# Kernel tuning notes

Measured on AMD Instinct MI355X. Metric: run time of the kernel, lower is better.

The kernel has to match this reference:

```python
import jax, jax.numpy as jnp
import numpy as np

D_MODEL = 512
H = 8
DEPTH = D_MODEL // H
TOPK = 16
TAU_HID = max(4, D_MODEL // 2)  # 256
TAU_EPS = 1e-6
DT = 1.0
T_SCALAR = 1.0  # default t in call()


def setup_inputs() -> dict:
    key = jax.random.key(0)
    ks = jax.random.split(key, 24)
    B, T = 2, 1024
    D2 = 2 * DEPTH

    def w(k, shape, fan_in):
        return jax.random.normal(k, shape, dtype=jnp.float32) / np.sqrt(fan_in)

    inp = {
        "x": jax.random.normal(ks[0], (B, T, D_MODEL), dtype=jnp.float32),
        "Wq": w(ks[1], (D_MODEL, D_MODEL), D_MODEL), "bq": jnp.zeros((D_MODEL,), jnp.float32),
        "Wk": w(ks[2], (D_MODEL, D_MODEL), D_MODEL), "bk": jnp.zeros((D_MODEL,), jnp.float32),
        "Wv": w(ks[3], (D_MODEL, D_MODEL), D_MODEL), "bv": jnp.zeros((D_MODEL,), jnp.float32),
        "Wo": w(ks[4], (D_MODEL, D_MODEL), D_MODEL), "bo": jnp.zeros((D_MODEL,), jnp.float32),
        "Wpi": w(ks[5], (D2, D_MODEL), D2), "bpi": jnp.zeros((D_MODEL,), jnp.float32),
        "Wpo": w(ks[6], (D_MODEL, 1), D_MODEL), "bpo": jnp.zeros((1,), jnp.float32),
        "Wta": w(ks[7], (D2, 1), D2), "bta": jnp.zeros((1,), jnp.float32),
        "Wtb": w(ks[8], (D2, 1), D2), "btb": jnp.zeros((1,), jnp.float32),
        "Wti": w(ks[9], (D2, TAU_HID), D2), "bti": jnp.zeros((TAU_HID,), jnp.float32),
        "Wto": w(ks[10], (TAU_HID, 1), TAU_HID), "bto": jnp.zeros((1,), jnp.float32),
    }
    return inp


def reference(x, Wq, bq, Wk, bk, Wv, bv, Wo, bo,
              Wpi, bpi, Wpo, bpo, Wta, bta, Wtb, btb, Wti, bti, Wto, bto):
    B, T, _ = x.shape

    def split_heads(z):
        return z.reshape(B, T, H, DEPTH).transpose(0, 2, 1, 3)  # [B,H,T,D]

    qh = split_heads(x @ Wq + bq)
    kh = split_heads(x @ Wk + bk)
    vh = split_heads(x @ Wv + bv)

    # top-k pairwise scores (q @ k^T), select K keys per query
    scores = jnp.einsum('bhqd,bhkd->bhqk', qh, kh)  # [B,H,T,T]
    _, idx = jax.lax.top_k(scores, TOPK)            # [B,H,T,K]

    # gather k and v at top-k indices -> [B,H,T,K,D]
    kg = jnp.take_along_axis(kh[:, :, None, :, :], idx[..., None], axis=3)
    vg = jnp.take_along_axis(vh[:, :, None, :, :], idx[..., None], axis=3)

    # per-pair features [q_i ; k_j] -> [B,H,T,K,2D]
    qt = jnp.broadcast_to(qh[:, :, :, None, :], (B, H, T, TOPK, DEPTH))
    pairs = jnp.concatenate([qt, kg], axis=-1)

    # phi: Dense(d_model) -> Dense(1) -> sigmoid
    phi = jax.nn.sigmoid(((pairs @ Wpi + bpi) @ Wpo + bpo)[..., 0])
    # time interpolation: sigmoid(a*t + b)
    t_a = (pairs @ Wta + bta)[..., 0]
    t_b = (pairs @ Wtb + btb)[..., 0]
    t_interp = jax.nn.sigmoid(t_a * T_SCALAR + t_b)
    # tau: Dense(d_model//2) -> Dense(1) -> softplus + eps
    tau = jax.nn.softplus(((pairs @ Wti + bti) @ Wto + bto)[..., 0]) + TAU_EPS

    # mode == 'exact'
    attn_logits = phi / tau * (1.0 - jnp.exp(-tau * t_interp))
    attn = jax.nn.softmax(attn_logits, axis=-1)  # [B,H,T,K]

    out_h = jnp.einsum('bhqk,bhqkd->bhqd', attn, vg) * DT  # [B,H,T,D]
    combined = out_h.transpose(0, 2, 1, 3).reshape(B, T, D_MODEL)
    return combined @ Wo + bo  # return_sequences=True
```

## Files before the change

kernel.cpp:

```cpp
#include <hip/hip_runtime.h>
#include <math.h>

#define BDIM 2
#define TT 1024
#define NH 8
#define HD 64
#define NTOPK 16
#define NBH 16
#define NTOK 16384

__global__ __launch_bounds__(256) void k_collapse64(
    const float* __restrict__ Wpi, const float* __restrict__ bpi,
    const float* __restrict__ Wpo, const float* __restrict__ bpo,
    const float* __restrict__ Wti, const float* __restrict__ bti,
    const float* __restrict__ Wto, const float* __restrict__ bto,
    double* __restrict__ wphid, double* __restrict__ wtaud,
    double* __restrict__ ccd) {
  int tid = threadIdx.x;
  int blk = blockIdx.x;
  if (blk < 16) {
    int r = blk * 16 + (tid >> 4);
    int l = tid & 15;
    double s = 0.;
    if (r < 128) {
      for (int i = 0; i < 32; ++i)
        s += (double)Wpi[r * 512 + l + 16 * i] * (double)Wpo[l + 16 * i];
    } else {
      int rr = r - 128;
      for (int i = 0; i < 16; ++i)
        s += (double)Wti[rr * 256 + l + 16 * i] * (double)Wto[l + 16 * i];
    }
#pragma unroll
    for (int off = 8; off >= 1; off >>= 1) s += __shfl_xor(s, off, 64);
    if (l == 0) {
      if (r < 128) wphid[r] = s;
      else wtaud[r - 128] = s;
    }
  } else {
    int lane = tid & 63;
    if (tid < 64) {
      double p = 0.;
      for (int c = lane; c < 512; c += 64) p += (double)bpi[c] * (double)Wpo[c];
#pragma unroll
      for (int off = 32; off >= 1; off >>= 1) p += __shfl_xor(p, off, 64);
      if (lane == 0) ccd[0] = p + (double)bpo[0];
    } else if (tid < 128) {
      double p = 0.;
      for (int c = lane; c < 256; c += 64) p += (double)bti[c] * (double)Wto[c];
#pragma unroll
      for (int off = 32; off >= 1; off >>= 1) p += __shfl_xor(p, off, 64);
      if (lane == 0) ccd[1] = p + (double)bto[0];
    }
  }
}

__device__ __forceinline__ void gemm_body(
    const float* __restrict__ A, const float* __restrict__ W,
    const float* __restrict__ bias, float* __restrict__ out,
    int bm, int bn, int mode) {
  __shared__ float As[32][68];
  __shared__ float Bs[32][64];
  const int tid = threadIdx.x;
  const int tx = tid & 15;
  const int ty = tid >> 4;
  float acc[4][4] = {{0.f, 0.f, 0.f, 0.f}};
  for (int k0 = 0; k0 < 512; k0 += 32) {
#pragma unroll
    for (int i = 0; i < 2; ++i) {
      int idx = i * 256 + tid;
      int row = idx >> 3;
      int c4 = (idx & 7) << 2;
      int sw = (idx & 7) << 3;
      int rs = row ^ sw;
      float4 av = *(const float4*)&A[(bm + row) * 512 + k0 + c4];
      As[c4 + 0][rs] = av.x;
      As[c4 + 1][rs] = av.y;
      As[c4 + 2][rs] = av.z;
      As[c4 + 3][rs] = av.w;
    }
#pragma unroll
    for (int i = 0; i < 2; ++i) {
      int idx = i * 256 + tid;
      int br = idx >> 4;
      int bc = (idx & 15) << 2;
      *(float4*)&Bs[br][bc] = *(const float4*)&W[(k0 + br) * 512 + bn + bc];
    }
    __syncthreads();
#pragma unroll
    for (int kk = 0; kk < 32; ++kk) {
      const int sr = ((kk >> 2) & 7) << 3;
      float4 a = *(const float4*)&As[kk][(ty * 4) ^ sr];
      float4 b = *(const float4*)&Bs[kk][tx << 2];
      acc[0][0] = fmaf(a.x, b.x, acc[0][0]);
      acc[0][1] = fmaf(a.x, b.y, acc[0][1]);
      acc[0][2] = fmaf(a.x, b.z, acc[0][2]);
      acc[0][3] = fmaf(a.x, b.w, acc[0][3]);
      acc[1][0] = fmaf(a.y, b.x, acc[1][0]);
      acc[1][1] = fmaf(a.y, b.y, acc[1][1]);
      acc[1][2] = fmaf(a.y, b.z, acc[1][2]);
      acc[1][3] = fmaf(a.y, b.w, acc[1][3]);
      acc[2][0] = fmaf(a.z, b.x, acc[2][0]);
      acc[2][1] = fmaf(a.z, b.y, acc[2][1]);
      acc[2][2] = fmaf(a.z, b.z, acc[2][2]);
      acc[2][3] = fmaf(a.z, b.w, acc[2][3]);
      acc[3][0] = fmaf(a.w, b.x, acc[3][0]);
      acc[3][1] = fmaf(a.w, b.y, acc[3][1]);
      acc[3][2] = fmaf(a.w, b.z, acc[3][2]);
      acc[3][3] = fmaf(a.w, b.w, acc[3][3]);
    }
    __syncthreads();
  }
#pragma unroll
  for (int i = 0; i < 4; ++i) {
    int row = bm + ty * 4 + i;
    float4 r;
    r.x = acc[i][0] + bias[bn + tx * 4 + 0];
    r.y = acc[i][1] + bias[bn + tx * 4 + 1];
    r.z = acc[i][2] + bias[bn + tx * 4 + 2];
    r.w = acc[i][3] + bias[bn + tx * 4 + 3];
    if (mode == 0) {
      *(float4*)&out[row * 512 + bn + tx * 4] = r;
    } else {
      int bb = row >> 10;
      int tt2 = row & 1023;
      int head = bn >> 6;
      *(float4*)&out[(((bb * NH + head) * TT + tt2) << 6) + tx * 4] = r;
    }
  }
}

__global__ __launch_bounds__(256) void k_gemm(
    const float* __restrict__ A, const float* __restrict__ W,
    const float* __restrict__ bias, float* __restrict__ out, int mode) {
  gemm_body(A, W, bias, out, blockIdx.y * 64, blockIdx.x * 64, mode);
}

__global__ __launch_bounds__(256) void k_gemm_qkv(
    const float* __restrict__ A,
    const float* __restrict__ Wq, const float* __restrict__ bq,
    const float* __restrict__ Wk, const float* __restrict__ bk,
    const float* __restrict__ Wv, const float* __restrict__ bv,
    float* __restrict__ Qf, float* __restrict__ Kf, float* __restrict__ Vf) {
  int which = blockIdx.x >> 3;
  int bn = (blockIdx.x & 7) * 64;
  const float* W = (which == 0) ? Wq : (which == 1) ? Wk : Wv;
  const float* b = (which == 0) ? bq : (which == 1) ? bk : bv;
  float* out = (which == 0) ? Qf : (which == 1) ? Kf : Vf;
  gemm_body(A, W, b, out, blockIdx.y * 64, bn, 1);
}

__global__ __launch_bounds__(256) void k_tokscal64(
    const float* __restrict__ Qg, const float* __restrict__ Kg,
    const double* __restrict__ wphid, const float* __restrict__ Wta,
    const float* __restrict__ Wtb, const double* __restrict__ wtaud,
    double4* __restrict__ sqd4, double4* __restrict__ skd4) {
  __shared__ double wp[128], wa[128], wb[128], wt[128];
  __shared__ float Qs[128][64];
  __shared__ float Ks[128][64];
  const int tid = threadIdx.x;
  if (tid < 128) {
    wp[tid] = wphid[tid];
    wa[tid] = (double)Wta[tid];
    wb[tid] = (double)Wtb[tid];
    wt[tid] = wtaud[tid];
  }
  const int tok0 = blockIdx.x * 128;
#pragma unroll
  for (int i = 0; i < 8; ++i) {
    int idx = i * 256 + tid;
    int row = idx >> 4;
    int c4 = (idx & 15) << 2;
    *(float4*)&Qs[row][c4] = *(const float4*)&Qg[(size_t)(tok0 + row) * 64 + c4];
    *(float4*)&Ks[row][c4] = *(const float4*)&Kg[(size_t)(tok0 + row) * 64 + c4];
  }
  __syncthreads();
  const int r = tid >> 1;
  const int h = tid & 1;
  const int dbase = h << 5;
  double sp = 0., sa = 0., sb = 0., st = 0.;
  double kp = 0., ka = 0., kb2 = 0., kt = 0.;
#pragma unroll
  for (int i = 0; i < 32; ++i) {
    int d = dbase + ((i + r) & 31);
    double q = (double)Qs[r][d];
    double k = (double)Ks[r][d];
    sp += q * wp[d];
    sa += q * wa[d];
    sb += q * wb[d];
    st += q * wt[d];
    kp += k * wp[64 + d];
    ka += k * wa[64 + d];
    kb2 += k * wb[64 + d];
    kt += k * wt[64 + d];
  }
  sp += __shfl_xor(sp, 1, 64);  sa += __shfl_xor(sa, 1, 64);
  sb += __shfl_xor(sb, 1, 64);  st += __shfl_xor(st, 1, 64);
  kp += __shfl_xor(kp, 1, 64);  ka += __shfl_xor(ka, 1, 64);
  kb2 += __shfl_xor(kb2, 1, 64); kt += __shfl_xor(kt, 1, 64);
  const int tok = tok0 + r;
  if (h == 0) sqd4[tok] = make_double4(sp, sa, sb, st);
  else        skd4[tok] = make_double4(kp, ka, kb2, kt);
}

__global__ __launch_bounds__(256) void k_score(
    const float* __restrict__ Qf, const float* __restrict__ Kf,
    float* __restrict__ Sc) {
  __shared__ float As[32][132];
  __shared__ float Bs[32][132];
  const int bn = blockIdx.x * 128;
  const int bm = blockIdx.y * 128;
  const int bh = blockIdx.z;
  const float* A = Qf + (size_t)bh * (TT * 64);
  const float* K = Kf + (size_t)bh * (TT * 64);
  float* out = Sc + (size_t)bh * (TT * 1024);
  const int tid = threadIdx.x;
  const int tx = tid & 15;
  const int ty = tid >> 4;
  float acc[8][8];
#pragma unroll
  for (int i = 0; i < 8; ++i)
#pragma unroll
    for (int j = 0; j < 8; ++j) acc[i][j] = 0.f;
  for (int k0 = 0; k0 < 64; k0 += 32) {
#pragma unroll
    for (int i = 0; i < 4; ++i) {
      int idx = i * 256 + tid;
      int row = idx >> 3;
      int c4 = (idx & 7) << 2;
      int sw = (idx & 7) << 3;
      int rs = row ^ sw;
      float4 av = *(const float4*)&A[(size_t)(bm + row) * 64 + k0 + c4];
      As[c4 + 0][rs] = av.x;
      As[c4 + 1][rs] = av.y;
      As[c4 + 2][rs] = av.z;
      As[c4 + 3][rs] = av.w;
      float4 kv = *(const float4*)&K[(size_t)(bn + row) * 64 + k0 + c4];
      Bs[c4 + 0][rs] = kv.x;
      Bs[c4 + 1][rs] = kv.y;
      Bs[c4 + 2][rs] = kv.z;
      Bs[c4 + 3][rs] = kv.w;
    }
    __syncthreads();
#pragma unroll
    for (int kk = 0; kk < 32; ++kk) {
      const int sr = ((kk >> 2) & 7) << 3;
      const int abase = (ty * 8) ^ sr;
      const int bbase = (tx * 8) ^ sr;
      float4 alo = *(const float4*)&As[kk][abase];
      float4 ahi = *(const float4*)&As[kk][abase + 4];
      float4 blo = *(const float4*)&Bs[kk][bbase];
      float4 bhi = *(const float4*)&Bs[kk][bbase + 4];
      float a[8] = {alo.x, alo.y, alo.z, alo.w, ahi.x, ahi.y, ahi.z, ahi.w};
      float b[8] = {blo.x, blo.y, blo.z, blo.w, bhi.x, bhi.y, bhi.z, bhi.w};
#pragma unroll
      for (int i = 0; i < 8; ++i)
#pragma unroll
        for (int j = 0; j < 8; ++j)
          acc[i][j] = fmaf(a[i], b[j], acc[i][j]);
    }
    __syncthreads();
  }
#pragma unroll
  for (int i = 0; i < 8; ++i) {
    float4 r0 = make_float4(acc[i][0], acc[i][1], acc[i][2], acc[i][3]);
    float4 r1 = make_float4(acc[i][4], acc[i][5], acc[i][6], acc[i][7]);
    size_t base = (size_t)(bm + ty * 8 + i) * 1024 + bn + tx * 8;
    *(float4*)&out[base] = r0;
    *(float4*)&out[base + 4] = r1;
  }
}

__global__ __launch_bounds__(256) void k_topk(
    const float* __restrict__ Sc, const float* __restrict__ Vg,
    const double4* __restrict__ sqd4, const double4* __restrict__ skd4,
    const double* __restrict__ ccd, const float* __restrict__ btaP,
    const float* __restrict__ btbP, float* __restrict__ C) {
  const int tid = threadIdx.x;
  const int lane = tid & 63;
  const int wv = tid >> 6;
  const int qg = blockIdx.x * 4 + wv;
  const int bh = qg >> 10;
  const int qa = qg & 1023;
  const int bb = bh >> 3;
  const int hh = bh & 7;
  const float* rowp = Sc + (size_t)qg * 1024;
  const float* Vbh = Vg + (size_t)bh * (TT * 64);
  float v[16];
#pragma unroll
  for (int g = 0; g < 4; ++g) {
    float4 t = *(const float4*)&rowp[g * 256 + lane * 4];
    v[g * 4 + 0] = t.x;
    v[g * 4 + 1] = t.y;
    v[g * 4 + 2] = t.z;
    v[g * 4 + 3] = t.w;
  }
  float gv[4];
  int gi[4];
  const int lbase = lane << 2;
#pragma unroll
  for (int g = 0; g < 4; ++g) {
    float nv = v[4 * g];
    int ne = 0;
#pragma unroll
    for (int e = 1; e < 4; ++e) {
      if (v[4 * g + e] > nv) { nv = v[4 * g + e]; ne = e; }
    }
    gv[g] = nv;
    gi[g] = (g << 8) | lbase | ne;
  }
  int myk = 0;
#pragma unroll 1
  for (int it = 0; it < NTOPK; ++it) {
    float cv = gv[0];
    int ci = gi[0];
#pragma unroll
    for (int g = 1; g < 4; ++g) {
      if (gv[g] > cv) { cv = gv[g]; ci = gi[g]; }
    }
    float M = cv;
#pragma unroll
    for (int off = 32; off >= 1; off >>= 1)
      M = fmaxf(M, __shfl_xor(M, off, 64));
    unsigned long long tied = __ballot(cv == M);
    int J;
    if (__popcll(tied) == 1) {
      int src = __ffsll(tied) - 1;
      J = __builtin_amdgcn_readfirstlane(__shfl(ci, src, 64));
    } else {
      int cj = (cv == M) ? ci : 0x7FFFFFFF;
#pragma unroll
      for (int off = 32; off >= 1; off >>= 1) {
        int oj = __shfl_xor(cj, off, 64);
        cj = (oj < cj) ? oj : cj;
      }
      J = __builtin_amdgcn_readfirstlane(cj);
    }
    if (lane == it) myk = J;
    const int owner = (J >> 2) & 63;
    const int g2 = J >> 8;
    const int e2 = J & 3;
    const bool isown = (lane == owner);
#pragma unroll
    for (int g = 0; g < 4; ++g) {
      if (g == g2) {
#pragma unroll
        for (int e = 0; e < 4; ++e) {
          if (e == e2) v[4 * g + e] = isown ? -INFINITY : v[4 * g + e];
        }
        float nv = v[4 * g];
        int ne = 0;
#pragma unroll
        for (int e = 1; e < 4; ++e) {
          if (v[4 * g + e] > nv) { nv = v[4 * g + e]; ne = e; }
        }
        gv[g] = nv;
        gi[g] = (g << 8) | lbase | ne;
      }
    }
  }
  const double cphi = ccd[0];
  const double ctau = ccd[1];
  const double bta0 = (double)btaP[0];
  const double btb0 = (double)btbP[0];
  double4 sq = sqd4[qg];
  float logit = -INFINITY;
  if (lane < 16) {
    double4 sk = skd4[bh * TT + myk];
    float xs = (float)(sq.x + sk.x + cphi);
    float ta = (float)(sq.y + sk.y + bta0);
    float tb = (float)(sq.z + sk.z + btb0);
    float tl = (float)(sq.w + sk.w + ctau);
    float phi = 1.f / (1.f + __expf(-xs));
    float ti = 1.f / (1.f + __expf(-(ta + tb)));
    float tau = fmaxf(tl, 0.f) + log1pf(__expf(-fabsf(tl))) + 1e-6f;
    logit = phi / tau * (1.f - __expf(-tau * ti));
  }
  float m = logit;
#pragma unroll
  for (int off = 8; off >= 1; off >>= 1) m = fmaxf(m, __shfl_xor(m, off, 64));
  float e = (lane < 16) ? __expf(logit - m) : 0.f;
  float ssum = e;
#pragma unroll
  for (int off = 8; off >= 1; off >>= 1) ssum += __shfl_xor(ssum, off, 64);
  float w = e / ssum;
  float outv = 0.f;
#pragma unroll
  for (int k2 = 0; k2 < NTOPK; ++k2) {
    float wk = __shfl(w, k2, 64);
    int ik = __shfl(myk, k2, 64);
    outv = fmaf(wk, Vbh[(size_t)ik * 64 + lane], outv);
  }
  C[(bb * TT + qa) * 512 + hh * 64 + lane] = outv;
}

__global__ __launch_bounds__(256) void k_attn_f(
    const float* __restrict__ Qg, const float* __restrict__ Kg,
    const float* __restrict__ Vg, const double4* __restrict__ sqd4,
    const double4* __restrict__ skd4, const double* __restrict__ ccd,
    const float* __restrict__ btaP, const float* __restrict__ btbP,
    float* __restrict__ C) {
  __shared__ float qs[8][64];
  __shared__ float sc[8][1024];
  const int bh = blockIdx.y;
  const int q0 = blockIdx.x * 8;
  const int tid = threadIdx.x;
  const int lane = tid & 63;
  const int wv = tid >> 6;
  if (tid < 128) {
    int q = tid >> 4, d4 = (tid & 15) << 2;
    *(float4*)&qs[q][d4] = *(const float4*)&Qg[(size_t)(bh * TT + q0 + q) * 64 + d4];
  }
  __syncthreads();
#pragma unroll 1
  for (int c = 0; c < 4; ++c) {
    const int kb = (c * 4 + wv) * 64;
    const float* krow = &Kg[(size_t)(bh * TT + kb + lane) * 64];
    float4 kr[16];
#pragma unroll
    for (int i = 0; i < 16; ++i) kr[i] = *(const float4*)&krow[i * 4];
#pragma unroll
    for (int q = 0; q < 8; ++q) {
      float s = 0.f;
#pragma unroll
      for (int i = 0; i < 16; ++i) {
        float4 q4 = *(const float4*)&qs[q][i * 4];
        s = fmaf(q4.x, kr[i].x, s);
        s = fmaf(q4.y, kr[i].y, s);
        s = fmaf(q4.z, kr[i].z, s);
        s = fmaf(q4.w, kr[i].w, s);
      }
      sc[q][kb + lane] = s;
    }
  }
  __syncthreads();
  const double cphi = ccd[0];
  const double ctau = ccd[1];
  const double bta0 = (double)btaP[0];
  const double btb0 = (double)btbP[0];
  const int bb = bh >> 3;
  const int hh = bh & 7;
  const float* Vbh = Vg + (size_t)bh * (TT * 64);
#pragma unroll 1
  for (int qq = 0; qq < 2; ++qq) {
    const int ql = wv * 2 + qq;
    const int qa = q0 + ql;
    float v[16];
#pragma unroll
    for (int jj = 0; jj < 16; ++jj) v[jj] = sc[ql][jj * 64 + lane];
    float gv[4];
    int gi[4];
#pragma unroll
    for (int g = 0; g < 4; ++g) {
      float nv = v[4 * g];
      int ne = 0;
#pragma unroll
      for (int e = 1; e < 4; ++e) {
        if (v[4 * g + e] > nv) { nv = v[4 * g + e]; ne = e; }
      }
      gv[g] = nv;
      gi[g] = ((4 * g + ne) << 6) | lane;
    }
    int myk = 0;
#pragma unroll 1
    for (int it = 0; it < NTOPK; ++it) {
      float cv = gv[0];
      int ci = gi[0];
#pragma unroll
      for (int g = 1; g < 4; ++g) {
        if (gv[g] > cv) { cv = gv[g]; ci = gi[g]; }
      }
      float M = cv;
#pragma unroll
      for (int off = 32; off >= 1; off >>= 1)
        M = fmaxf(M, __shfl_xor(M, off, 64));
      unsigned long long tied = __ballot(cv == M);
      int J;
      if (__popcll(tied) == 1) {
        int src = __ffsll(tied) - 1;
        J = __builtin_amdgcn_readfirstlane(__shfl(ci, src, 64));
      } else {
        int cj = (cv == M) ? ci : 0x7FFFFFFF;
#pragma unroll
        for (int off = 32; off >= 1; off >>= 1) {
          int oj = __shfl_xor(cj, off, 64);
          cj = (oj < cj) ? oj : cj;
        }
        J = __builtin_amdgcn_readfirstlane(cj);
      }
      if (lane == it) myk = J;
      const int owner = J & 63;
      const int slot2 = J >> 6;
      const int g2 = slot2 >> 2;
      const int e2 = slot2 & 3;
      const bool isown = (lane == owner);
#pragma unroll
      for (int g = 0; g < 4; ++g) {
        if (g == g2) {
#pragma unroll
          for (int e = 0; e < 4; ++e) {
            if (e == e2) v[4 * g + e] = isown ? -INFINITY : v[4 * g + e];
          }
          float nv = v[4 * g];
          int ne = 0;
#pragma unroll
          for (int e = 1; e < 4; ++e) {
            if (v[4 * g + e] > nv) { nv = v[4 * g + e]; ne = e; }
          }
          gv[g] = nv;
          gi[g] = ((4 * g + ne) << 6) | lane;
        }
      }
    }
    double4 sq = sqd4[(size_t)bh * TT + qa];
    float logit = -INFINITY;
    if (lane < 16) {
      double4 sk = skd4[bh * TT + myk];
      float xs = (float)(sq.x + sk.x + cphi);
      float ta = (float)(sq.y + sk.y + bta0);
      float tb = (float)(sq.z + sk.z + btb0);
      float tl = (float)(sq.w + sk.w + ctau);
      float phi = 1.f / (1.f + __expf(-xs));
      float ti = 1.f / (1.f + __expf(-(ta + tb)));
      float tau = fmaxf(tl, 0.f) + log1pf(__expf(-fabsf(tl))) + 1e-6f;
      logit = phi / tau * (1.f - __expf(-tau * ti));
    }
    float m = logit;
#pragma unroll
    for (int off = 8; off >= 1; off >>= 1) m = fmaxf(m, __shfl_xor(m, off, 64));
    float e = (lane < 16) ? __expf(logit - m) : 0.f;
    float ssum = e;
#pragma unroll
    for (int off = 8; off >= 1; off >>= 1) ssum += __shfl_xor(ssum, off, 64);
    float w = e / ssum;
    float outv = 0.f;
#pragma unroll
    for (int k2 = 0; k2 < NTOPK; ++k2) {
      float wk = __shfl(w, k2, 64);
      int ik = __shfl(myk, k2, 64);
      outv = fmaf(wk, Vbh[(size_t)ik * 64 + lane], outv);
    }
    C[(bb * TT + qa) * 512 + hh * 64 + lane] = outv;
  }
}

extern "C" void kernel_launch(void* const* d_in, const int* in_sizes, int n_in,
                              void* d_out, int out_size, void* d_ws, size_t ws_size,
                              hipStream_t stream) {
  (void)in_sizes; (void)n_in; (void)out_size;
  const float* x   = (const float*)d_in[0];
  const float* Wq  = (const float*)d_in[1];
  const float* bq  = (const float*)d_in[2];
  const float* Wk  = (const float*)d_in[3];
  const float* bk  = (const float*)d_in[4];
  const float* Wv  = (const float*)d_in[5];
  const float* bv  = (const float*)d_in[6];
  const float* Wo  = (const float*)d_in[7];
  const float* bo  = (const float*)d_in[8];
  const float* Wpi = (const float*)d_in[9];
  const float* bpi = (const float*)d_in[10];
  const float* Wpo = (const float*)d_in[11];
  const float* bpo = (const float*)d_in[12];
  const float* Wta = (const float*)d_in[13];
  const float* bta = (const float*)d_in[14];
  const float* Wtb = (const float*)d_in[15];
  const float* btb = (const float*)d_in[16];
  const float* Wti = (const float*)d_in[17];
  const float* bti = (const float*)d_in[18];
  const float* Wto = (const float*)d_in[19];
  const float* bto = (const float*)d_in[20];

  double* wsd = (double*)d_ws;
  double4* sqd4 = (double4*)wsd;
  double4* skd4 = (double4*)(wsd + 65536);
  double* wphid = wsd + 131072;
  double* wtaud = wsd + 131200;
  double* ccd   = wsd + 131328;
  float* fs = (float*)(wsd + 131332);
  float* Qf = fs;
  float* Kf = fs + 1048576;
  float* Vf = fs + 2097152;
  float* Cf = fs + 3145728;
  float* Sc = fs + 4194304;
  const size_t need = (size_t)131332 * 8 + (size_t)(4194304 + 16777216) * 4;

  hipLaunchKernelGGL(k_collapse64, dim3(17), dim3(256), 0, stream,
                     Wpi, bpi, Wpo, bpo, Wti, bti, Wto, bto, wphid, wtaud, ccd);
  hipLaunchKernelGGL(k_gemm_qkv, dim3(24, 32), dim3(256), 0, stream,
                     x, Wq, bq, Wk, bk, Wv, bv, Qf, Kf, Vf);
  hipLaunchKernelGGL(k_tokscal64, dim3(NTOK / 128), dim3(256), 0, stream,
                     Qf, Kf, wphid, Wta, Wtb, wtaud, sqd4, skd4);
  if (ws_size >= need) {
    hipLaunchKernelGGL(k_score, dim3(8, 8, 16), dim3(256), 0, stream, Qf, Kf, Sc);
    hipLaunchKernelGGL(k_topk, dim3(NTOK / 4), dim3(256), 0, stream,
                       Sc, Vf, sqd4, skd4, ccd, bta, btb, Cf);
  } else {
    hipLaunchKernelGGL(k_attn_f, dim3(TT / 8, NBH), dim3(256), 0, stream,
                       Qf, Kf, Vf, sqd4, skd4, ccd, bta, btb, Cf);
  }
  hipLaunchKernelGGL(k_gemm, dim3(8, 32), dim3(256), 0, stream,
                     Cf, Wo, bo, (float*)d_out, 0);
}
```

Measured before the change: 244.4 us.

## Fuse score GEMM and top-k into one register-resident attention kernel

Replaces the separate score GEMM (which wrote a full 16x1024x1024 score matrix to global memory) and the top-k kernel with one fused kernel. Each block computes scores for 32 queries against K tiles staged transposed in shared memory, keeping each wave's 8 query rows of scores in registers, then runs top-k selection and the softmax/V reduction directly. This removes the 64 MB score write and read-back, at the cost of heavy register pressure from the 128-float per-thread score array and fewer blocks (512).

```diff
diff --git a/kernel.cpp b/kernel.cpp
--- a/kernel.cpp
+++ b/kernel.cpp
@@ -202,237 +202,82 @@
   else        skd4[tok] = make_double4(kp, ka, kb2, kt);
 }
 
-__global__ __launch_bounds__(256) void k_score(
-    const float* __restrict__ Qf, const float* __restrict__ Kf,
-    float* __restrict__ Sc) {
-  __shared__ float As[32][132];
-  __shared__ float Bs[32][132];
-  const int bn = blockIdx.x * 128;
-  const int bm = blockIdx.y * 128;
-  const int bh = blockIdx.z;
-  const float* A = Qf + (size_t)bh * (TT * 64);
-  const float* K = Kf + (size_t)bh * (TT * 64);
-  float* out = Sc + (size_t)bh * (TT * 1024);
-  const int tid = threadIdx.x;
-  const int tx = tid & 15;
-  const int ty = tid >> 4;
-  float acc[8][8];
-#pragma unroll
-  for (int i = 0; i < 8; ++i)
-#pragma unroll
-    for (int j = 0; j < 8; ++j) acc[i][j] = 0.f;
-  for (int k0 = 0; k0 < 64; k0 += 32) {
-#pragma unroll
-    for (int i = 0; i < 4; ++i) {
-      int idx = i * 256 + tid;
-      int row = idx >> 3;
-      int c4 = (idx & 7) << 2;
-      int sw = (idx & 7) << 3;
-      int rs = row ^ sw;
-      float4 av = *(const float4*)&A[(size_t)(bm + row) * 64 + k0 + c4];
-      As[c4 + 0][rs] = av.x;
-      As[c4 + 1][rs] = av.y;
-      As[c4 + 2][rs] = av.z;
-      As[c4 + 3][rs] = av.w;
-      float4 kv = *(const float4*)&K[(size_t)(bn + row) * 64 + k0 + c4];
-      Bs[c4 + 0][rs] = kv.x;
-      Bs[c4 + 1][rs] = kv.y;
-      Bs[c4 + 2][rs] = kv.z;
-      Bs[c4 + 3][rs] = kv.w;
-    }
-    __syncthreads();
-#pragma unroll
-    for (int kk = 0; kk < 32; ++kk) {
-      const int sr = ((kk >> 2) & 7) << 3;
-      const int abase = (ty * 8) ^ sr;
-      const int bbase = (tx * 8) ^ sr;
-      float4 alo = *(const float4*)&As[kk][abase];
-      float4 ahi = *(const float4*)&As[kk][abase + 4];
-      float4 blo = *(const float4*)&Bs[kk][bbase];
-      float4 bhi = *(const float4*)&Bs[kk][bbase + 4];
-      float a[8] = {alo.x, alo.y, alo.z, alo.w, ahi.x, ahi.y, ahi.z, ahi.w};
-      float b[8] = {blo.x, blo.y, blo.z, blo.w, bhi.x, bhi.y, bhi.z, bhi.w};
-#pragma unroll
-      for (int i = 0; i < 8; ++i)
-#pragma unroll
-        for (int j = 0; j < 8; ++j)
-          acc[i][j] = fmaf(a[i], b[j], acc[i][j]);
-    }
-    __syncthreads();
-  }
-#pragma unroll
-  for (int i = 0; i < 8; ++i) {
-    float4 r0 = make_float4(acc[i][0], acc[i][1], acc[i][2], acc[i][3]);
-    float4 r1 = make_float4(acc[i][4], acc[i][5], acc[i][6], acc[i][7]);
-    size_t base = (size_t)(bm + ty * 8 + i) * 1024 + bn + tx * 8;
-    *(float4*)&out[base] = r0;
-    *(float4*)&out[base + 4] = r1;
-  }
-}
-
-__global__ __launch_bounds__(256) void k_topk(
-    const float* __restrict__ Sc, const float* __restrict__ Vg,
-    const double4* __restrict__ sqd4, const double4* __restrict__ skd4,
-    const double* __restrict__ ccd, const float* __restrict__ btaP,
-    const float* __restrict__ btbP, float* __restrict__ C) {
-  const int tid = threadIdx.x;
-  const int lane = tid & 63;
-  const int wv = tid >> 6;
-  const int qg = blockIdx.x * 4 + wv;
-  const int bh = qg >> 10;
-  const int qa = qg & 1023;
-  const int bb = bh >> 3;
-  const int hh = bh & 7;
-  const float* rowp = Sc + (size_t)qg * 1024;
-  const float* Vbh = Vg + (size_t)bh * (TT * 64);
-  float v[16];
-#pragma unroll
-  for (int g = 0; g < 4; ++g) {
-    float4 t = *(const float4*)&rowp[g * 256 + lane * 4];
-    v[g * 4 + 0] = t.x;
-    v[g * 4 + 1] = t.y;
-    v[g * 4 + 2] = t.z;
-    v[g * 4 + 3] = t.w;
-  }
-  float gv[4];
-  int gi[4];
-  const int lbase = lane << 2;
-#pragma unroll
-  for (int g = 0; g < 4; ++g) {
-    float nv = v[4 * g];
-    int ne = 0;
-#pragma unroll
-    for (int e = 1; e < 4; ++e) {
-      if (v[4 * g + e] > nv) { nv = v[4 * g + e]; ne = e; }
-    }
-    gv[g] = nv;
-    gi[g] = (g << 8) | lbase | ne;
-  }
-  int myk = 0;
-#pragma unroll 1
-  for (int it = 0; it < NTOPK; ++it) {
-    float cv = gv[0];
-    int ci = gi[0];
-#pragma unroll
-    for (int g = 1; g < 4; ++g) {
-      if (gv[g] > cv) { cv = gv[g]; ci = gi[g]; }
-    }
-    float M = cv;
-#pragma unroll
-    for (int off = 32; off >= 1; off >>= 1)
-      M = fmaxf(M, __shfl_xor(M, off, 64));
-    unsigned long long tied = __ballot(cv == M);
-    int J;
-    if (__popcll(tied) == 1) {
-      int src = __ffsll(tied) - 1;
-      J = __builtin_amdgcn_readfirstlane(__shfl(ci, src, 64));
-    } else {
-      int cj = (cv == M) ? ci : 0x7FFFFFFF;
-#pragma unroll
-      for (int off = 32; off >= 1; off >>= 1) {
-        int oj = __shfl_xor(cj, off, 64);
-        cj = (oj < cj) ? oj : cj;
-      }
-      J = __builtin_amdgcn_readfirstlane(cj);
-    }
-    if (lane == it) myk = J;
-    const int owner = (J >> 2) & 63;
-    const int g2 = J >> 8;
-    const int e2 = J & 3;
-    const bool isown = (lane == owner);
-#pragma unroll
-    for (int g = 0; g < 4; ++g) {
-      if (g == g2) {
-#pragma unroll
-        for (int e = 0; e < 4; ++e) {
-          if (e == e2) v[4 * g + e] = isown ? -INFINITY : v[4 * g + e];
-        }
-        float nv = v[4 * g];
-        int ne = 0;
-#pragma unroll
-        for (int e = 1; e < 4; ++e) {
-          if (v[4 * g + e] > nv) { nv = v[4 * g + e]; ne = e; }
-        }
-        gv[g] = nv;
-        gi[g] = (g << 8) | lbase | ne;
-      }
-    }
-  }
-  const double cphi = ccd[0];
-  const double ctau = ccd[1];
-  const double bta0 = (double)btaP[0];
-  const double btb0 = (double)btbP[0];
-  double4 sq = sqd4[qg];
-  float logit = -INFINITY;
-  if (lane < 16) {
-    double4 sk = skd4[bh * TT + myk];
-    float xs = (float)(sq.x + sk.x + cphi);
-    float ta = (float)(sq.y + sk.y + bta0);
-    float tb = (float)(sq.z + sk.z + btb0);
-    float tl = (float)(sq.w + sk.w + ctau);
-    float phi = 1.f / (1.f + __expf(-xs));
-    float ti = 1.f / (1.f + __expf(-(ta + tb)));
-    float tau = fmaxf(tl, 0.f) + log1pf(__expf(-fabsf(tl))) + 1e-6f;
-    logit = phi / tau * (1.f - __expf(-tau * ti));
-  }
-  float m = logit;
-#pragma unroll
-  for (int off = 8; off >= 1; off >>= 1) m = fmaxf(m, __shfl_xor(m, off, 64));
-  float e = (lane < 16) ? __expf(logit - m) : 0.f;
-  float ssum = e;
-#pragma unroll
-  for (int off = 8; off >= 1; off >>= 1) ssum += __shfl_xor(ssum, off, 64);
-  float w = e / ssum;
-  float outv = 0.f;
-#pragma unroll
-  for (int k2 = 0; k2 < NTOPK; ++k2) {
-    float wk = __shfl(w, k2, 64);
-    int ik = __shfl(myk, k2, 64);
-    outv = fmaf(wk, Vbh[(size_t)ik * 64 + lane], outv);
-  }
-  C[(bb * TT + qa) * 512 + hh * 64 + lane] = outv;
-}
-
-__global__ __launch_bounds__(256) void k_attn_f(
+__global__ __launch_bounds__(256) void k_attn_f3(
     const float* __restrict__ Qg, const float* __restrict__ Kg,
     const float* __restrict__ Vg, const double4* __restrict__ sqd4,
     const double4* __restrict__ skd4, const double* __restrict__ ccd,
     const float* __restrict__ btaP, const float* __restrict__ btbP,
     float* __restrict__ C) {
-  __shared__ float qs[8][64];
-  __shared__ float sc[8][1024];
+  __shared__ float qs[32][64];
+  __shared__ float KT[64][260];
   const int bh = blockIdx.y;
-  const int q0 = blockIdx.x * 8;
+  const int q0 = blockIdx.x * 32;
   const int tid = threadIdx.x;
   const int lane = tid & 63;
   const int wv = tid >> 6;
-  if (tid < 128) {
-    int q = tid >> 4, d4 = (tid & 15) << 2;
-    *(float4*)&qs[q][d4] = *(const float4*)&Qg[(size_t)(bh * TT + q0 + q) * 64 + d4];
-  }
-  __syncthreads();
+
+#pragma unroll
+  for (int i = 0; i < 2; ++i) {
+    int idx = i * 256 + tid;
+    int row = idx >> 4;
+    int c4 = (idx & 15) << 2;
+    *(float4*)&qs[row][c4] =
+        *(const float4*)&Qg[(size_t)(bh * TT + q0 + row) * 64 + c4];
+  }
+
+  float v[8][16];
+#pragma unroll
+  for (int r = 0; r < 8; ++r)
+#pragma unroll
+    for (int s = 0; s < 16; ++s) v[r][s] = 0.f;
+
+#pragma unroll
+  for (int t = 0; t < 4; ++t) {
+    __syncthreads();
+#pragma unroll
+    for (int i = 0; i < 16; ++i) {
+      int idx = i * 256 + tid;
+      int kr = idx >> 4;
+      int d4 = (idx & 15) << 2;
+      float4 kv =
+          *(const float4*)&Kg[(size_t)(bh * TT + t * 256 + kr) * 64 + d4];
+      int krs = kr ^ (((d4 >> 2) & 7) << 3);
+      KT[d4 + 0][krs] = kv.x;
+      KT[d4 + 1][krs] = kv.y;
+      KT[d4 + 2][krs] = kv.z;
+      KT[d4 + 3][krs] = kv.w;
+    }
+    __syncthreads();
 #pragma unroll 1
-  for (int c = 0; c < 4; ++c) {
-    const int kb = (c * 4 + wv) * 64;
-    const float* krow = &Kg[(size_t)(bh * TT + kb + lane) * 64];
-    float4 kr[16];
-#pragma unroll
-    for (int i = 0; i < 16; ++i) kr[i] = *(const float4*)&krow[i * 4];
-#pragma unroll
-    for (int q = 0; q < 8; ++q) {
-      float s = 0.f;
-#pragma unroll
-      for (int i = 0; i < 16; ++i) {
-        float4 q4 = *(const float4*)&qs[q][i * 4];
-        s = fmaf(q4.x, kr[i].x, s);
-        s = fmaf(q4.y, kr[i].y, s);
-        s = fmaf(q4.z, kr[i].z, s);
-        s = fmaf(q4.w, kr[i].w, s);
+    for (int d4 = 0; d4 < 64; d4 += 4) {
+      const int cbase = (lane << 2) ^ (((d4 >> 2) & 7) << 3);
+      float4 k0 = *(const float4*)&KT[d4 + 0][cbase];
+      float4 k1 = *(const float4*)&KT[d4 + 1][cbase];
+      float4 k2 = *(const float4*)&KT[d4 + 2][cbase];
+      float4 k3 = *(const float4*)&KT[d4 + 3][cbase];
+#pragma unroll
+      for (int r = 0; r < 8; ++r) {
+        float4 q4 = *(const float4*)&qs[wv * 8 + r][d4];
+        v[r][t * 4 + 0] = fmaf(q4.x, k0.x, v[r][t * 4 + 0]);
+        v[r][t * 4 + 1] = fmaf(q4.x, k0.y, v[r][t * 4 + 1]);
+        v[r][t * 4 + 2] = fmaf(q4.x, k0.z, v[r][t * 4 + 2]);
+        v[r][t * 4 + 3] = fmaf(q4.x, k0.w, v[r][t * 4 + 3]);
+        v[r][t * 4 + 0] = fmaf(q4.y, k1.x, v[r][t * 4 + 0]);
+        v[r][t * 4 + 1] = fmaf(q4.y, k1.y, v[r][t * 4 + 1]);
+        v[r][t * 4 + 2] = fmaf(q4.y, k1.z, v[r][t * 4 + 2]);
+        v[r][t * 4 + 3] = fmaf(q4.y, k1.w, v[r][t * 4 + 3]);
+        v[r][t * 4 + 0] = fmaf(q4.z, k2.x, v[r][t * 4 + 0]);
+        v[r][t * 4 + 1] = fmaf(q4.z, k2.y, v[r][t * 4 + 1]);
+        v[r][t * 4 + 2] = fmaf(q4.z, k2.z, v[r][t * 4 + 2]);
+        v[r][t * 4 + 3] = fmaf(q4.z, k2.w, v[r][t * 4 + 3]);
+        v[r][t * 4 + 0] = fmaf(q4.w, k3.x, v[r][t * 4 + 0]);
+        v[r][t * 4 + 1] = fmaf(q4.w, k3.y, v[r][t * 4 + 1]);
+        v[r][t * 4 + 2] = fmaf(q4.w, k3.z, v[r][t * 4 + 2]);
+        v[r][t * 4 + 3] = fmaf(q4.w, k3.w, v[r][t * 4 + 3]);
       }
-      sc[q][kb + lane] = s;
-    }
-  }
-  __syncthreads();
+    }
+  }
+
   const double cphi = ccd[0];
   const double ctau = ccd[1];
   const double bta0 = (double)btaP[0];
@@ -440,25 +285,22 @@
   const int bb = bh >> 3;
   const int hh = bh & 7;
   const float* Vbh = Vg + (size_t)bh * (TT * 64);
-#pragma unroll 1
-  for (int qq = 0; qq < 2; ++qq) {
-    const int ql = wv * 2 + qq;
-    const int qa = q0 + ql;
-    float v[16];
-#pragma unroll
-    for (int jj = 0; jj < 16; ++jj) v[jj] = sc[ql][jj * 64 + lane];
+  const int lbase = lane << 2;
+#pragma unroll
+  for (int r = 0; r < 8; ++r) {
+    const int qa = q0 + wv * 8 + r;
     float gv[4];
     int gi[4];
 #pragma unroll
     for (int g = 0; g < 4; ++g) {
-      float nv = v[4 * g];
+      float nv = v[r][4 * g];
       int ne = 0;
 #pragma unroll
       for (int e = 1; e < 4; ++e) {
-        if (v[4 * g + e] > nv) { nv = v[4 * g + e]; ne = e; }
+        if (v[r][4 * g + e] > nv) { nv = v[r][4 * g + e]; ne = e; }
       }
       gv[g] = nv;
-      gi[g] = ((4 * g + ne) << 6) | lane;
+      gi[g] = (g << 8) | lbase | ne;
     }
     int myk = 0;
 #pragma unroll 1
@@ -488,26 +330,25 @@
         J = __builtin_amdgcn_readfirstlane(cj);
       }
       if (lane == it) myk = J;
-      const int owner = J & 63;
-      const int slot2 = J >> 6;
-      const int g2 = slot2 >> 2;
-      const int e2 = slot2 & 3;
+      const int owner = (J >> 2) & 63;
+      const int g2 = J >> 8;
+      const int e2 = J & 3;
       const bool isown = (lane == owner);
 #pragma unroll
       for (int g = 0; g < 4; ++g) {
         if (g == g2) {
 #pragma unroll
           for (int e = 0; e < 4; ++e) {
-            if (e == e2) v[4 * g + e] = isown ? -INFINITY : v[4 * g + e];
+            if (e == e2) v[r][4 * g + e] = isown ? -INFINITY : v[r][4 * g + e];
           }
-          float nv = v[4 * g];
+          float nv = v[r][4 * g];
           int ne = 0;
 #pragma unroll
           for (int e = 1; e < 4; ++e) {
-            if (v[4 * g + e] > nv) { nv = v[4 * g + e]; ne = e; }
+            if (v[r][4 * g + e] > nv) { nv = v[r][4 * g + e]; ne = e; }
           }
           gv[g] = nv;
-          gi[g] = ((4 * g + ne) << 6) | lane;
+          gi[g] = (g << 8) | lbase | ne;
         }
       }
     }
@@ -546,7 +387,7 @@
 extern "C" void kernel_launch(void* const* d_in, const int* in_sizes, int n_in,
                               void* d_out, int out_size, void* d_ws, size_t ws_size,
                               hipStream_t stream) {
-  (void)in_sizes; (void)n_in; (void)out_size;
+  (void)in_sizes; (void)n_in; (void)out_size; (void)ws_size;
   const float* x   = (const float*)d_in[0];
   const float* Wq  = (const float*)d_in[1];
   const float* bq  = (const float*)d_in[2];
@@ -580,8 +421,6 @@
   float* Kf = fs + 1048576;
   float* Vf = fs + 2097152;
   float* Cf = fs + 3145728;
-  float* Sc = fs + 4194304;
-  const size_t need = (size_t)131332 * 8 + (size_t)(4194304 + 16777216) * 4;
 
   hipLaunchKernelGGL(k_collapse64, dim3(17), dim3(256), 0, stream,
                      Wpi, bpi, Wpo, bpo, Wti, bti, Wto, bto, wphid, wtaud, ccd);
@@ -589,14 +428,8 @@
                      x, Wq, bq, Wk, bk, Wv, bv, Qf, Kf, Vf);
   hipLaunchKernelGGL(k_tokscal64, dim3(NTOK / 128), dim3(256), 0, stream,
                      Qf, Kf, wphid, Wta, Wtb, wtaud, sqd4, skd4);
-  if (ws_size >= need) {
-    hipLaunchKernelGGL(k_score, dim3(8, 8, 16), dim3(256), 0, stream, Qf, Kf, Sc);
-    hipLaunchKernelGGL(k_topk, dim3(NTOK / 4), dim3(256), 0, stream,
-                       Sc, Vf, sqd4, skd4, ccd, bta, btb, Cf);
-  } else {
-    hipLaunchKernelGGL(k_attn_f, dim3(TT / 8, NBH), dim3(256), 0, stream,
-                       Qf, Kf, Vf, sqd4, skd4, ccd, bta, btb, Cf);
-  }
+  hipLaunchKernelGGL(k_attn_f3, dim3(32, NBH), dim3(256), 0, stream,
+                     Qf, Kf, Vf, sqd4, skd4, ccd, bta, btb, Cf);
   hipLaunchKernelGGL(k_gemm, dim3(8, 32), dim3(256), 0, stream,
                      Cf, Wo, bo, (float*)d_out, 0);
 }
```

New measurement: 277.5 us. 1.14x slower.
